# Kernel optimization log

Hardware: AMD Instinct MI355X
Metric: run time of the kernel (lower is better)

## Reference

```python
import jax, jax.numpy as jnp
import numpy as np

B, S, D, H = 2, 2048, 1024, 16
HD = D // H  # head_dim = 64


def setup_inputs() -> dict:
    key = jax.random.key(0)
    ks = jax.random.split(key, 5)
    scale = 1.0 / np.sqrt(D)
    return {
        "x": jax.random.normal(ks[0], (B, S, D), dtype=jnp.float32),
        "attention_mask": jnp.zeros((B, 1, 1, S), dtype=jnp.float32),
        "Wq": jax.random.normal(ks[1], (D, D), dtype=jnp.float32) * scale,
        "Wk": jax.random.normal(ks[2], (D, D), dtype=jnp.float32) * scale,
        "Wv": jax.random.normal(ks[3], (D, D), dtype=jnp.float32) * scale,
        "Wo": jax.random.normal(ks[4], (D, D), dtype=jnp.float32) * scale,
    }


def reference(x, attention_mask, Wq, Wk, Wv, Wo):
    # nn.Linear applies x @ W.T; weights here stored as [out, in]
    q = jnp.einsum("bsd,ed->bse", x, Wq).reshape(B, S, H, HD).transpose(0, 2, 1, 3)
    k = jnp.einsum("bsd,ed->bse", x, Wk).reshape(B, S, H, HD).transpose(0, 2, 1, 3)
    v = jnp.einsum("bsd,ed->bse", x, Wv).reshape(B, S, H, HD).transpose(0, 2, 1, 3)
    scores = jnp.einsum("bhqd,bhkd->bhqk", q, k) / jnp.sqrt(jnp.float32(HD))
    scores = scores + attention_mask  # additive mask, broadcasts [B,1,1,S]
    attn = jax.nn.softmax(scores, axis=-1)  # dropout p=0 (eval) -> identity
    ctx = jnp.einsum("bhqk,bhkd->bhqd", attn, v)
    ctx = ctx.transpose(0, 2, 1, 3).reshape(B, S, D)
    out = jnp.einsum("bsd,ed->bse", ctx, Wo)
    return out
```

## Files before the change

kernel.cpp:

```cpp
#include <hip/hip_runtime.h>
#include <hip/hip_bf16.h>
#include <cstdint>
#include <cstddef>


#define B_  2
#define S_  2048
#define D_  1024
#define H_  16
#define HD_ 64

typedef __bf16 bf16x8 __attribute__((ext_vector_type(8)));
typedef __bf16 bf16x4 __attribute__((ext_vector_type(4)));
typedef float  f32x4  __attribute__((ext_vector_type(4)));

__device__ __forceinline__ void async16(const __bf16* g, const __bf16* l) {
  __builtin_amdgcn_global_load_lds(
      (const __attribute__((address_space(1))) void*)(uintptr_t)g,
      (__attribute__((address_space(3))) void*)(uint32_t)(uintptr_t)l,
      16, 0, 0);
}

__device__ __forceinline__ unsigned cvt_pk_bf16(float lo, float hi) {
  unsigned r;
  asm("v_cvt_pk_bf16_f32 %0, %1, %2" : "=v"(r) : "v"(lo), "v"(hi));
  return r;
}

__global__ __launch_bounds__(256) void cvt_all(const float* __restrict__ x,
    const float* __restrict__ wq, const float* __restrict__ wk,
    const float* __restrict__ wv, const float* __restrict__ wo,
    __bf16* __restrict__ xb, __bf16* __restrict__ wqb, __bf16* __restrict__ wkb,
    __bf16* __restrict__ wvb, __bf16* __restrict__ wob) {
  const int sel = blockIdx.y;
  const float* src; __bf16* dst; int n;
  if      (sel == 0) { src = x;  dst = xb;  n = B_ * S_ * D_; }
  else if (sel == 1) { src = wq; dst = wqb; n = D_ * D_; }
  else if (sel == 2) { src = wk; dst = wkb; n = D_ * D_; }
  else if (sel == 3) { src = wv; dst = wvb; n = D_ * D_; }
  else               { src = wo; dst = wob; n = D_ * D_; }
  for (int i = blockIdx.x * 256 + threadIdx.x; i * 4 < n; i += gridDim.x * 256) {
    const float4 v = *(const float4*)(src + (size_t)i * 4);
    bf16x4 o;
    o[0] = (__bf16)v.x; o[1] = (__bf16)v.y; o[2] = (__bf16)v.z; o[3] = (__bf16)v.w;
    *(bf16x4*)(dst + (size_t)i * 4) = o;
  }
}

__global__ __launch_bounds__(512, 4) void qkv_gemm(const __bf16* __restrict__ xb,
                                                   const __bf16* __restrict__ wqkv,
                                                   __bf16* __restrict__ qkv) {
  __shared__ __align__(16) char smem[65536];
  __bf16* cs = (__bf16*)smem;

  const int lin = blockIdx.y * 24 + blockIdx.x;
  const int xcd = lin & 7, slot = lin >> 3;
  const int mi = xcd >> 2, ni = xcd & 3;
  const int mB = mi * 16 + slot / 6;
  const int nB = ni * 6  + slot % 6;
  const int m0  = mB * 128;
  const int sel = nB >> 3;
  const int n0s = (nB & 7) * 128;
  const int n0w = nB * 128;
  constexpr int K = D_, N = D_;
  constexpr size_t NTE = (size_t)B_ * S_ * D_;

  const int tid  = threadIdx.x, lane = tid & 63, wave = tid >> 6;
  const int l15  = lane & 15,   quad = lane >> 4;
  const int wr   = wave >> 1,   wc   = wave & 1;

  const int e0 = (wave * 2 + 0) * 512 + lane * 8;
  const int e1 = (wave * 2 + 1) * 512 + lane * 8;
  const int r0 = e0 >> 6, c0 = e0 & 63, r1 = e1 >> 6, c1 = e1 & 63;

  f32x4 acc[2][4] = {};

  {
    __bf16* As = (__bf16*)(smem);
    __bf16* Bs = (__bf16*)(smem + 16384);
    async16(xb   + (size_t)(m0  + r0) * K + c0, As + (wave * 2 + 0) * 512);
    async16(xb   + (size_t)(m0  + r1) * K + c1, As + (wave * 2 + 1) * 512);
    async16(wqkv + (size_t)(n0w + r0) * K + c0, Bs + (wave * 2 + 0) * 512);
    async16(wqkv + (size_t)(n0w + r1) * K + c1, Bs + (wave * 2 + 1) * 512);
  }
  __syncthreads();

  for (int t = 0; t < K / 64; ++t) {
    const int cur = t & 1;
    if (t + 1 < K / 64) {
      const int k0 = (t + 1) * 64;
      __bf16* As = (__bf16*)(smem + (cur ^ 1) * 32768);
      __bf16* Bs = (__bf16*)(smem + (cur ^ 1) * 32768 + 16384);
      async16(xb   + (size_t)(m0  + r0) * K + k0 + c0, As + (wave * 2 + 0) * 512);
      async16(xb   + (size_t)(m0  + r1) * K + k0 + c1, As + (wave * 2 + 1) * 512);
      async16(wqkv + (size_t)(n0w + r0) * K + k0 + c0, Bs + (wave * 2 + 0) * 512);
      async16(wqkv + (size_t)(n0w + r1) * K + k0 + c1, Bs + (wave * 2 + 1) * 512);
    }
    const __bf16* As = (const __bf16*)(smem + cur * 32768);
    const __bf16* Bs = (const __bf16*)(smem + cur * 32768 + 16384);
#pragma unroll
    for (int kk = 0; kk < 2; ++kk) {
      bf16x8 af[2], bfv[4];
#pragma unroll
      for (int rt = 0; rt < 2; ++rt)
        af[rt] = *(const bf16x8*)(As + (wr * 32 + rt * 16 + l15) * 64 + kk * 32 + quad * 8);
#pragma unroll
      for (int ct = 0; ct < 4; ++ct)
        bfv[ct] = *(const bf16x8*)(Bs + (wc * 64 + ct * 16 + l15) * 64 + kk * 32 + quad * 8);
#pragma unroll
      for (int rt = 0; rt < 2; ++rt)
#pragma unroll
        for (int ct = 0; ct < 4; ++ct)
          acc[rt][ct] = __builtin_amdgcn_mfma_f32_16x16x32_bf16(af[rt], bfv[ct], acc[rt][ct], 0, 0, 0);
    }
    __syncthreads();
  }

  const int b  = m0 >> 11;
  const int s0 = m0 & (S_ - 1);
  __bf16* vtb = qkv + 2 * NTE;
#pragma unroll
  for (int pass = 0; pass < 2; ++pass) {
    __syncthreads();
    if ((wave >> 2) == pass) {
#pragma unroll
      for (int rt = 0; rt < 2; ++rt)
#pragma unroll
        for (int ct = 0; ct < 4; ++ct)
#pragma unroll
          for (int r = 0; r < 4; ++r)
            cs[((wr & 1) * 32 + rt * 16 + quad * 4 + r) * 136 + wc * 64 + ct * 16 + l15] =
                (__bf16)acc[rt][ct][r];
    }
    __syncthreads();
    if (sel < 2) {
      __bf16* C = qkv + (size_t)sel * NTE;
      const int rr = tid >> 3, cb = (tid & 7) * 16;
      const bf16x8 v0 = *(const bf16x8*)(cs + rr * 136 + cb);
      const bf16x8 v1 = *(const bf16x8*)(cs + rr * 136 + cb + 8);
      *(bf16x8*)(C + (size_t)(m0 + pass * 64 + rr) * N + n0s + cb)     = v0;
      *(bf16x8*)(C + (size_t)(m0 + pass * 64 + rr) * N + n0s + cb + 8) = v1;
    } else {
      const int e_loc = tid >> 2, sh = (tid & 3) * 16;
      __bf16* dst = vtb + (size_t)(b * 1024 + n0s + e_loc) * S_ + s0 + pass * 64 + sh;
#pragma unroll
      for (int p2 = 0; p2 < 2; ++p2) {
        bf16x8 v;
#pragma unroll
        for (int j = 0; j < 8; ++j)
          v[j] = cs[(sh + p2 * 8 + j) * 136 + e_loc];
        *(bf16x8*)(dst + p2 * 8) = v;
      }
    }
  }
}

__global__ __launch_bounds__(512, 4) void o_gemm(const __bf16* __restrict__ cb,
                                                 const __bf16* __restrict__ wo,
                                                 float* __restrict__ out) {
  __shared__ __align__(16) char smem[49152];
  const int lin = blockIdx.y * 8 + blockIdx.x;
  const int xcd = lin & 7, slot = lin >> 3;
  const int mi = xcd >> 1, ni = xcd & 1;
  const int mB = mi * 16 + (slot >> 2);
  const int nB = ni * 4  + (slot & 3);
  const int m0 = mB * 64, n0 = nB * 128;
  constexpr int K = D_, N = D_;
  const int tid  = threadIdx.x, lane = tid & 63, wave = tid >> 6;
  const int l15  = lane & 15,   quad = lane >> 4;
  const int wr   = wave >> 2,   wc   = wave & 3;

  const int ea  = wave * 512 + lane * 8;
  const int ra  = ea >> 6, ca = ea & 63;
  const int eb0 = (wave * 2 + 0) * 512 + lane * 8;
  const int eb1 = (wave * 2 + 1) * 512 + lane * 8;
  const int rb0 = eb0 >> 6, cb0 = eb0 & 63, rb1 = eb1 >> 6, cb1 = eb1 & 63;

  f32x4 acc[2][2] = {};
  {
    __bf16* As = (__bf16*)(smem);
    __bf16* Bs = (__bf16*)(smem + 8192);
    async16(cb + (size_t)(m0 + ra)  * K + ca,  As + wave * 512);
    async16(wo + (size_t)(n0 + rb0) * K + cb0, Bs + (wave * 2 + 0) * 512);
    async16(wo + (size_t)(n0 + rb1) * K + cb1, Bs + (wave * 2 + 1) * 512);
  }
  __syncthreads();

  for (int t = 0; t < K / 64; ++t) {
    const int cur = t & 1;
    if (t + 1 < K / 64) {
      const int k0 = (t + 1) * 64;
      __bf16* As = (__bf16*)(smem + (cur ^ 1) * 24576);
      __bf16* Bs = (__bf16*)(smem + (cur ^ 1) * 24576 + 8192);
      async16(cb + (size_t)(m0 + ra)  * K + k0 + ca,  As + wave * 512);
      async16(wo + (size_t)(n0 + rb0) * K + k0 + cb0, Bs + (wave * 2 + 0) * 512);
      async16(wo + (size_t)(n0 + rb1) * K + k0 + cb1, Bs + (wave * 2 + 1) * 512);
    }
    const __bf16* As = (const __bf16*)(smem + cur * 24576);
    const __bf16* Bs = (const __bf16*)(smem + cur * 24576 + 8192);
#pragma unroll
    for (int kk = 0; kk < 2; ++kk) {
      bf16x8 af[2], bfv[2];
#pragma unroll
      for (int rt = 0; rt < 2; ++rt)
        af[rt] = *(const bf16x8*)(As + (wr * 32 + rt * 16 + l15) * 64 + kk * 32 + quad * 8);
#pragma unroll
      for (int ct = 0; ct < 2; ++ct)
        bfv[ct] = *(const bf16x8*)(Bs + (wc * 32 + ct * 16 + l15) * 64 + kk * 32 + quad * 8);
#pragma unroll
      for (int rt = 0; rt < 2; ++rt)
#pragma unroll
        for (int ct = 0; ct < 2; ++ct)
          acc[rt][ct] = __builtin_amdgcn_mfma_f32_16x16x32_bf16(af[rt], bfv[ct], acc[rt][ct], 0, 0, 0);
    }
    __syncthreads();
  }
#pragma unroll
  for (int rt = 0; rt < 2; ++rt)
#pragma unroll
    for (int ct = 0; ct < 2; ++ct)
#pragma unroll
      for (int r = 0; r < 4; ++r) {
        const int row = m0 + wr * 32 + rt * 16 + quad * 4 + r;
        const int col = n0 + wc * 32 + ct * 16 + l15;
        out[(size_t)row * N + col] = acc[rt][ct][r];
      }
}

__global__ __launch_bounds__(512, 4) void attn2(const __bf16* __restrict__ Q,
                                                const __bf16* __restrict__ K,
                                                const __bf16* __restrict__ Vt,
                                                const float* __restrict__ mask,
                                                __bf16* __restrict__ O) {
  constexpr int LKT = 72, LVT = 136;
  __shared__ __align__(16) __bf16 kt[2][128 * LKT];
  __shared__ __align__(16) __bf16 vt[2][64 * LVT];
  __shared__ __align__(16) float  mfull[S_];

  const int tid  = threadIdx.x, lane = tid & 63, wave = tid >> 6;
  const int l15  = lane & 15,   quad = lane >> 4;
  const int b = blockIdx.z, h = blockIdx.y, q0 = blockIdx.x * 128;
  const size_t base   = (size_t)b * S_ * D_ + h * HD_;
  const size_t vtbase = (size_t)(b * H_ + h) * HD_ * S_;
  const int qw = q0 + wave * 16;
  constexpr float LOG2E = 1.44269504088896340736f;
  constexpr float SC    = 0.125f * LOG2E;
  constexpr int  NT     = S_ / 128;

  const int idx0 = tid,        kr0 = idx0 >> 3, kc0 = (idx0 & 7) * 8;
  const int idx1 = 512 + tid,  kr1 = idx1 >> 3, kc1 = (idx1 & 7) * 8;
  const int vr0 = idx0 >> 4, vc0 = (idx0 & 15) * 8;
  const int vr1 = idx1 >> 4, vc1 = (idx1 & 15) * 8;

  bf16x8 qf[2];
#pragma unroll
  for (int kb = 0; kb < 2; ++kb)
    qf[kb] = *(const bf16x8*)(Q + base + (size_t)(qw + l15) * D_ + kb * 32 + quad * 8);

  bf16x8 ones;
#pragma unroll
  for (int j = 0; j < 8; ++j) ones[j] = (__bf16)1.0f;

  float m_run = -1e30f;
  f32x4 oacc[4] = {};
  f32x4 lacc   = {};

  bf16x8 rk0, rk1, rv0, rv1;
  rk0 = *(const bf16x8*)(K + base + (size_t)kr0 * D_ + kc0);
  rk1 = *(const bf16x8*)(K + base + (size_t)kr1 * D_ + kc1);
  rv0 = *(const bf16x8*)(Vt + vtbase + (size_t)vr0 * S_ + vc0);
  rv1 = *(const bf16x8*)(Vt + vtbase + (size_t)vr1 * S_ + vc1);
#pragma unroll
  for (int i = 0; i < S_ / 512; ++i)
    mfull[i * 512 + tid] = mask[(size_t)b * S_ + i * 512 + tid] * LOG2E;
  *(bf16x8*)(&kt[0][kr0 * LKT + kc0]) = rk0;
  *(bf16x8*)(&kt[0][kr1 * LKT + kc1]) = rk1;
  *(bf16x8*)(&vt[0][vr0 * LVT + vc0]) = rv0;
  *(bf16x8*)(&vt[0][vr1 * LVT + vc1]) = rv1;
  if (NT > 1) {
    rk0 = *(const bf16x8*)(K + base + (size_t)(128 + kr0) * D_ + kc0);
    rk1 = *(const bf16x8*)(K + base + (size_t)(128 + kr1) * D_ + kc1);
    rv0 = *(const bf16x8*)(Vt + vtbase + (size_t)vr0 * S_ + 128 + vc0);
    rv1 = *(const bf16x8*)(Vt + vtbase + (size_t)vr1 * S_ + 128 + vc1);
  }
  __syncthreads();

  for (int t = 0; t < NT; ++t) {
    const int cur = t & 1;
    const int t0  = t * 128;
    const __bf16* ktb = &kt[cur][0];
    const __bf16* vtb = &vt[cur][0];

    if (t + 1 < NT) {
      const int nxt = cur ^ 1;
      *(bf16x8*)(&kt[nxt][kr0 * LKT + kc0]) = rk0;
      *(bf16x8*)(&kt[nxt][kr1 * LKT + kc1]) = rk1;
      *(bf16x8*)(&vt[nxt][vr0 * LVT + vc0]) = rv0;
      *(bf16x8*)(&vt[nxt][vr1 * LVT + vc1]) = rv1;
    }
    if (t + 2 < NT) {
      const int tn = t0 + 256;
      rk0 = *(const bf16x8*)(K + base + (size_t)(tn + kr0) * D_ + kc0);
      rk1 = *(const bf16x8*)(K + base + (size_t)(tn + kr1) * D_ + kc1);
      rv0 = *(const bf16x8*)(Vt + vtbase + (size_t)vr0 * S_ + tn + vc0);
      rv1 = *(const bf16x8*)(Vt + vtbase + (size_t)vr1 * S_ + tn + vc1);
    }

    f32x4 sacc[8] = {};
    __builtin_amdgcn_s_setprio(1);
#pragma unroll
    for (int kti = 0; kti < 8; ++kti) {
      const __bf16* kr = ktb + (kti * 16 + l15) * LKT + quad * 8;
      const bf16x8 a0 = *(const bf16x8*)(kr);
      const bf16x8 a1 = *(const bf16x8*)(kr + 32);
      sacc[kti] = __builtin_amdgcn_mfma_f32_16x16x32_bf16(a0, qf[0], sacc[kti], 0, 0, 0);
      sacc[kti] = __builtin_amdgcn_mfma_f32_16x16x32_bf16(a1, qf[1], sacc[kti], 0, 0, 0);
    }
    __builtin_amdgcn_s_setprio(0);

    f32x4 tm4;
#pragma unroll
    for (int r = 0; r < 4; ++r) tm4[r] = -1e30f;
#pragma unroll
    for (int kti = 0; kti < 8; ++kti) {
      const f32x4 mv = *(const f32x4*)(mfull + t0 + kti * 16 + quad * 4);
#pragma unroll
      for (int r = 0; r < 4; ++r) {
        sacc[kti][r] = sacc[kti][r] * SC + mv[r];
        tm4[r] = fmaxf(tm4[r], sacc[kti][r]);
      }
    }
    float tm = fmaxf(fmaxf(tm4[0], tm4[1]), fmaxf(tm4[2], tm4[3]));
    tm = fmaxf(tm, __shfl_xor(tm, 16));
    tm = fmaxf(tm, __shfl_xor(tm, 32));

    if (!__all(tm <= m_run + 8.f)) {
      const float mnew  = fmaxf(m_run, tm);
      const float alpha = __builtin_amdgcn_exp2f(m_run - mnew);
      m_run = mnew;
#pragma unroll
      for (int r = 0; r < 4; ++r) {
        const float aR = __shfl(alpha, quad * 4 + r);
        lacc[r] *= aR;
#pragma unroll
        for (int nt = 0; nt < 4; ++nt) oacc[nt][r] *= aR;
      }
    }

#pragma unroll
    for (int kb = 0; kb < 4; ++kb) {
      unsigned dd[2][2];
#pragma unroll
      for (int kk = 0; kk < 2; ++kk) {
        const int kti = 2 * kb + kk;
        float p[4];
#pragma unroll
        for (int r = 0; r < 4; ++r)
          p[r] = __builtin_amdgcn_exp2f(sacc[kti][r] - m_run);
        dd[kk][0] = cvt_pk_bf16(p[0], p[1]);
        dd[kk][1] = cvt_pk_bf16(p[2], p[3]);
      }
      unsigned a0 = dd[0][0], b0 = dd[1][0], a1 = dd[0][1], b1 = dd[1][1];
      asm("v_permlane32_swap_b32 %0, %1" : "+v"(a0), "+v"(b0));
      asm("v_permlane16_swap_b32 %0, %1" : "+v"(a0), "+v"(b0));
      asm("v_permlane32_swap_b32 %0, %1" : "+v"(a1), "+v"(b1));
      asm("v_permlane16_swap_b32 %0, %1" : "+v"(a1), "+v"(b1));
      union { unsigned u[4]; bf16x8 v; } pw;
      pw.u[0] = a0; pw.u[1] = a1; pw.u[2] = b0; pw.u[3] = b1;
      const bf16x8 pa = pw.v;
      __builtin_amdgcn_s_setprio(1);
      lacc = __builtin_amdgcn_mfma_f32_16x16x32_bf16(pa, ones, lacc, 0, 0, 0);
#pragma unroll
      for (int nt = 0; nt < 4; ++nt) {
        const bf16x8 vf = *(const bf16x8*)(vtb + (nt * 16 + l15) * LVT + kb * 32 + quad * 8);
        oacc[nt] = __builtin_amdgcn_mfma_f32_16x16x32_bf16(pa, vf, oacc[nt], 0, 0, 0);
      }
      __builtin_amdgcn_s_setprio(0);
    }

    __syncthreads();
  }

#pragma unroll
  for (int r = 0; r < 4; ++r) {
    const float inv = 1.0f / lacc[r];
    const int row = qw + quad * 4 + r;
#pragma unroll
    for (int nt = 0; nt < 4; ++nt)
      O[base + (size_t)row * D_ + nt * 16 + l15] = (__bf16)(oacc[nt][r] * inv);
  }
}

extern "C" void kernel_launch(void* const* d_in, const int* in_sizes, int n_in,
                              void* d_out, int out_size, void* d_ws, size_t ws_size,
                              hipStream_t stream) {
  const float* x    = (const float*)d_in[0];
  const float* mask = (const float*)d_in[1];
  const float* Wq   = (const float*)d_in[2];
  const float* Wk   = (const float*)d_in[3];
  const float* Wv   = (const float*)d_in[4];
  const float* Wo   = (const float*)d_in[5];

  char* ws = (char*)d_ws;
  const size_t MB = 1ull << 20;
  const size_t NT = (size_t)B_ * S_ * D_;
  __bf16* xb  = (__bf16*)(ws);
  __bf16* wqb = (__bf16*)(ws + 8 * MB);
  __bf16* wkb = (__bf16*)(ws + 10 * MB);
  __bf16* wvb = (__bf16*)(ws + 12 * MB);
  __bf16* wob = (__bf16*)(ws + 14 * MB);
  __bf16* qkv = (__bf16*)(ws + 16 * MB);
  __bf16* qb  = qkv;
  __bf16* kb  = qkv + NT;
  __bf16* vtb = qkv + 2 * NT;
  __bf16* cb  = xb;

  cvt_all<<<dim3(1024, 5), 256, 0, stream>>>(x, Wq, Wk, Wv, Wo, xb, wqb, wkb, wvb, wob);
  qkv_gemm<<<dim3(24, 32), 512, 0, stream>>>(xb, wqb, qkv);
  attn2<<<dim3(S_ / 128, H_, B_), 512, 0, stream>>>(qb, kb, vtb, mask, cb);
  o_gemm<<<dim3(8, 64), 512, 0, stream>>>(cb, wob, (float*)d_out);
}
```

Baseline: 200.1 us.

## Enlarge QKV GEMM tiles to 256x256 and shrink o_gemm blocks to 256 threads

The QKV projection GEMM moves from 128x128 tiles on 768 blocks to 256x256 tiles on 192 blocks. It uses 128KB of LDS and each wave holds an 8x4 accumulator grid, which raises operand reuse per LDS load. The epilogue now writes out in four passes. o_gemm runs with 4 waves per block instead of 8, each wave covering a 32x64 output. Risks: only 192 blocks for 256 CUs, so many CUs sit idle, plus high register pressure and one block per CU with less latency hiding.

```diff
diff --git a/kernel.cpp b/kernel.cpp
--- a/kernel.cpp
+++ b/kernel.cpp
@@ -47,41 +47,38 @@
   }
 }
 
-__global__ __launch_bounds__(512, 4) void qkv_gemm(const __bf16* __restrict__ xb,
+__global__ __launch_bounds__(512, 1) void qkv_gemm(const __bf16* __restrict__ xb,
                                                    const __bf16* __restrict__ wqkv,
                                                    __bf16* __restrict__ qkv) {
-  __shared__ __align__(16) char smem[65536];
+  __shared__ __align__(16) char smem[131072];
   __bf16* cs = (__bf16*)smem;
 
-  const int lin = blockIdx.y * 24 + blockIdx.x;
+  const int lin = blockIdx.y * 12 + blockIdx.x;
   const int xcd = lin & 7, slot = lin >> 3;
-  const int mi = xcd >> 2, ni = xcd & 3;
-  const int mB = mi * 16 + slot / 6;
-  const int nB = ni * 6  + slot % 6;
-  const int m0  = mB * 128;
-  const int sel = nB >> 3;
-  const int n0s = (nB & 7) * 128;
-  const int n0w = nB * 128;
+  const int mB = (xcd >> 2) * 8 + slot / 3;
+  const int nB = (xcd & 3) * 3 + slot % 3;
+  const int m0  = mB * 256;
+  const int sel = nB >> 2;
+  const int n0s = (nB & 3) * 256;
+  const int n0w = nB * 256;
   constexpr int K = D_, N = D_;
   constexpr size_t NTE = (size_t)B_ * S_ * D_;
 
   const int tid  = threadIdx.x, lane = tid & 63, wave = tid >> 6;
   const int l15  = lane & 15,   quad = lane >> 4;
-  const int wr   = wave >> 1,   wc   = wave & 1;
-
-  const int e0 = (wave * 2 + 0) * 512 + lane * 8;
-  const int e1 = (wave * 2 + 1) * 512 + lane * 8;
-  const int r0 = e0 >> 6, c0 = e0 & 63, r1 = e1 >> 6, c1 = e1 & 63;
-
-  f32x4 acc[2][4] = {};
+  const int wr   = wave >> 2,   wc   = wave & 3;
+  const int row8 = tid >> 3, col8 = (tid & 7) * 8;
+
+  f32x4 acc[8][4] = {};
 
   {
     __bf16* As = (__bf16*)(smem);
-    __bf16* Bs = (__bf16*)(smem + 16384);
-    async16(xb   + (size_t)(m0  + r0) * K + c0, As + (wave * 2 + 0) * 512);
-    async16(xb   + (size_t)(m0  + r1) * K + c1, As + (wave * 2 + 1) * 512);
-    async16(wqkv + (size_t)(n0w + r0) * K + c0, Bs + (wave * 2 + 0) * 512);
-    async16(wqkv + (size_t)(n0w + r1) * K + c1, Bs + (wave * 2 + 1) * 512);
+    __bf16* Bs = (__bf16*)(smem + 32768);
+#pragma unroll
+    for (int i = 0; i < 4; ++i) {
+      async16(xb   + (size_t)(m0  + i * 64 + row8) * K + col8, As + i * 4096 + wave * 512);
+      async16(wqkv + (size_t)(n0w + i * 64 + row8) * K + col8, Bs + i * 4096 + wave * 512);
+    }
   }
   __syncthreads();
 
@@ -89,29 +86,29 @@
     const int cur = t & 1;
     if (t + 1 < K / 64) {
       const int k0 = (t + 1) * 64;
-      __bf16* As = (__bf16*)(smem + (cur ^ 1) * 32768);
-      __bf16* Bs = (__bf16*)(smem + (cur ^ 1) * 32768 + 16384);
-      async16(xb   + (size_t)(m0  + r0) * K + k0 + c0, As + (wave * 2 + 0) * 512);
-      async16(xb   + (size_t)(m0  + r1) * K + k0 + c1, As + (wave * 2 + 1) * 512);
-      async16(wqkv + (size_t)(n0w + r0) * K + k0 + c0, Bs + (wave * 2 + 0) * 512);
-      async16(wqkv + (size_t)(n0w + r1) * K + k0 + c1, Bs + (wave * 2 + 1) * 512);
-    }
-    const __bf16* As = (const __bf16*)(smem + cur * 32768);
-    const __bf16* Bs = (const __bf16*)(smem + cur * 32768 + 16384);
+      __bf16* As = (__bf16*)(smem + (cur ^ 1) * 65536);
+      __bf16* Bs = (__bf16*)(smem + (cur ^ 1) * 65536 + 32768);
+#pragma unroll
+      for (int i = 0; i < 4; ++i) {
+        async16(xb   + (size_t)(m0  + i * 64 + row8) * K + k0 + col8, As + i * 4096 + wave * 512);
+        async16(wqkv + (size_t)(n0w + i * 64 + row8) * K + k0 + col8, Bs + i * 4096 + wave * 512);
+      }
+    }
+    const __bf16* As = (const __bf16*)(smem + cur * 65536);
+    const __bf16* Bs = (const __bf16*)(smem + cur * 65536 + 32768);
 #pragma unroll
     for (int kk = 0; kk < 2; ++kk) {
-      bf16x8 af[2], bfv[4];
-#pragma unroll
-      for (int rt = 0; rt < 2; ++rt)
-        af[rt] = *(const bf16x8*)(As + (wr * 32 + rt * 16 + l15) * 64 + kk * 32 + quad * 8);
+      bf16x8 bfv[4];
 #pragma unroll
       for (int ct = 0; ct < 4; ++ct)
         bfv[ct] = *(const bf16x8*)(Bs + (wc * 64 + ct * 16 + l15) * 64 + kk * 32 + quad * 8);
 #pragma unroll
-      for (int rt = 0; rt < 2; ++rt)
+      for (int rt = 0; rt < 8; ++rt) {
+        const bf16x8 af = *(const bf16x8*)(As + (wr * 128 + rt * 16 + l15) * 64 + kk * 32 + quad * 8);
 #pragma unroll
         for (int ct = 0; ct < 4; ++ct)
-          acc[rt][ct] = __builtin_amdgcn_mfma_f32_16x16x32_bf16(af[rt], bfv[ct], acc[rt][ct], 0, 0, 0);
+          acc[rt][ct] = __builtin_amdgcn_mfma_f32_16x16x32_bf16(af, bfv[ct], acc[rt][ct], 0, 0, 0);
+      }
     }
     __syncthreads();
   }
@@ -120,44 +117,46 @@
   const int s0 = m0 & (S_ - 1);
   __bf16* vtb = qkv + 2 * NTE;
 #pragma unroll
-  for (int pass = 0; pass < 2; ++pass) {
+  for (int pass = 0; pass < 4; ++pass) {
     __syncthreads();
-    if ((wave >> 2) == pass) {
-#pragma unroll
-      for (int rt = 0; rt < 2; ++rt)
+    if (wr == (pass >> 1)) {
+      const int rtb = (pass & 1) * 4;
+#pragma unroll
+      for (int rt = 0; rt < 4; ++rt)
 #pragma unroll
         for (int ct = 0; ct < 4; ++ct)
 #pragma unroll
           for (int r = 0; r < 4; ++r)
-            cs[((wr & 1) * 32 + rt * 16 + quad * 4 + r) * 136 + wc * 64 + ct * 16 + l15] =
-                (__bf16)acc[rt][ct][r];
+            cs[(rt * 16 + quad * 4 + r) * 264 + wc * 64 + ct * 16 + l15] =
+                (__bf16)acc[rtb + rt][ct][r];
     }
     __syncthreads();
     if (sel < 2) {
       __bf16* C = qkv + (size_t)sel * NTE;
-      const int rr = tid >> 3, cb = (tid & 7) * 16;
-      const bf16x8 v0 = *(const bf16x8*)(cs + rr * 136 + cb);
-      const bf16x8 v1 = *(const bf16x8*)(cs + rr * 136 + cb + 8);
-      *(bf16x8*)(C + (size_t)(m0 + pass * 64 + rr) * N + n0s + cb)     = v0;
-      *(bf16x8*)(C + (size_t)(m0 + pass * 64 + rr) * N + n0s + cb + 8) = v1;
+      const int rr = tid >> 3, cb = (tid & 7) * 32;
+#pragma unroll
+      for (int j2 = 0; j2 < 4; ++j2) {
+        const bf16x8 v = *(const bf16x8*)(cs + rr * 264 + cb + j2 * 8);
+        *(bf16x8*)(C + (size_t)(m0 + pass * 64 + rr) * N + n0s + cb + j2 * 8) = v;
+      }
     } else {
-      const int e_loc = tid >> 2, sh = (tid & 3) * 16;
+      const int e_loc = tid >> 1, sh = (tid & 1) * 32;
       __bf16* dst = vtb + (size_t)(b * 1024 + n0s + e_loc) * S_ + s0 + pass * 64 + sh;
 #pragma unroll
-      for (int p2 = 0; p2 < 2; ++p2) {
+      for (int j2 = 0; j2 < 4; ++j2) {
         bf16x8 v;
 #pragma unroll
         for (int j = 0; j < 8; ++j)
-          v[j] = cs[(sh + p2 * 8 + j) * 136 + e_loc];
-        *(bf16x8*)(dst + p2 * 8) = v;
-      }
-    }
-  }
-}
-
-__global__ __launch_bounds__(512, 4) void o_gemm(const __bf16* __restrict__ cb,
-                                                 const __bf16* __restrict__ wo,
-                                                 float* __restrict__ out) {
+          v[j] = cs[(sh + j2 * 8 + j) * 264 + e_loc];
+        *(bf16x8*)(dst + j2 * 8) = v;
+      }
+    }
+  }
+}
+
+__global__ __launch_bounds__(256) void o_gemm(const __bf16* __restrict__ cb,
+                                              const __bf16* __restrict__ wo,
+                                              float* __restrict__ out) {
   __shared__ __align__(16) char smem[49152];
   const int lin = blockIdx.y * 8 + blockIdx.x;
   const int xcd = lin & 7, slot = lin >> 3;
@@ -168,21 +167,19 @@
   constexpr int K = D_, N = D_;
   const int tid  = threadIdx.x, lane = tid & 63, wave = tid >> 6;
   const int l15  = lane & 15,   quad = lane >> 4;
-  const int wr   = wave >> 2,   wc   = wave & 3;
-
-  const int ea  = wave * 512 + lane * 8;
-  const int ra  = ea >> 6, ca = ea & 63;
-  const int eb0 = (wave * 2 + 0) * 512 + lane * 8;
-  const int eb1 = (wave * 2 + 1) * 512 + lane * 8;
-  const int rb0 = eb0 >> 6, cb0 = eb0 & 63, rb1 = eb1 >> 6, cb1 = eb1 & 63;
-
-  f32x4 acc[2][2] = {};
+  const int wr   = wave >> 1,   wc   = wave & 1;
+  const int row8 = tid >> 3, col8 = (tid & 7) * 8;
+
+  f32x4 acc[2][4] = {};
   {
     __bf16* As = (__bf16*)(smem);
     __bf16* Bs = (__bf16*)(smem + 8192);
-    async16(cb + (size_t)(m0 + ra)  * K + ca,  As + wave * 512);
-    async16(wo + (size_t)(n0 + rb0) * K + cb0, Bs + (wave * 2 + 0) * 512);
-    async16(wo + (size_t)(n0 + rb1) * K + cb1, Bs + (wave * 2 + 1) * 512);
+#pragma unroll
+    for (int i = 0; i < 2; ++i)
+      async16(cb + (size_t)(m0 + i * 32 + row8) * K + col8, As + i * 2048 + wave * 512);
+#pragma unroll
+    for (int i = 0; i < 4; ++i)
+      async16(wo + (size_t)(n0 + i * 32 + row8) * K + col8, Bs + i * 2048 + wave * 512);
   }
   __syncthreads();
 
@@ -192,25 +189,28 @@
       const int k0 = (t + 1) * 64;
       __bf16* As = (__bf16*)(smem + (cur ^ 1) * 24576);
       __bf16* Bs = (__bf16*)(smem + (cur ^ 1) * 24576 + 8192);
-      async16(cb + (size_t)(m0 + ra)  * K + k0 + ca,  As + wave * 512);
-      async16(wo + (size_t)(n0 + rb0) * K + k0 + cb0, Bs + (wave * 2 + 0) * 512);
-      async16(wo + (size_t)(n0 + rb1) * K + k0 + cb1, Bs + (wave * 2 + 1) * 512);
+#pragma unroll
+      for (int i = 0; i < 2; ++i)
+        async16(cb + (size_t)(m0 + i * 32 + row8) * K + k0 + col8, As + i * 2048 + wave * 512);
+#pragma unroll
+      for (int i = 0; i < 4; ++i)
+        async16(wo + (size_t)(n0 + i * 32 + row8) * K + k0 + col8, Bs + i * 2048 + wave * 512);
     }
     const __bf16* As = (const __bf16*)(smem + cur * 24576);
     const __bf16* Bs = (const __bf16*)(smem + cur * 24576 + 8192);
 #pragma unroll
     for (int kk = 0; kk < 2; ++kk) {
-      bf16x8 af[2], bfv[2];
+      bf16x8 af[2], bfv[4];
 #pragma unroll
       for (int rt = 0; rt < 2; ++rt)
         af[rt] = *(const bf16x8*)(As + (wr * 32 + rt * 16 + l15) * 64 + kk * 32 + quad * 8);
 #pragma unroll
-      for (int ct = 0; ct < 2; ++ct)
-        bfv[ct] = *(const bf16x8*)(Bs + (wc * 32 + ct * 16 + l15) * 64 + kk * 32 + quad * 8);
+      for (int ct = 0; ct < 4; ++ct)
+        bfv[ct] = *(const bf16x8*)(Bs + (wc * 64 + ct * 16 + l15) * 64 + kk * 32 + quad * 8);
 #pragma unroll
       for (int rt = 0; rt < 2; ++rt)
 #pragma unroll
-        for (int ct = 0; ct < 2; ++ct)
+        for (int ct = 0; ct < 4; ++ct)
           acc[rt][ct] = __builtin_amdgcn_mfma_f32_16x16x32_bf16(af[rt], bfv[ct], acc[rt][ct], 0, 0, 0);
     }
     __syncthreads();
@@ -218,11 +218,11 @@
 #pragma unroll
   for (int rt = 0; rt < 2; ++rt)
 #pragma unroll
-    for (int ct = 0; ct < 2; ++ct)
+    for (int ct = 0; ct < 4; ++ct)
 #pragma unroll
       for (int r = 0; r < 4; ++r) {
         const int row = m0 + wr * 32 + rt * 16 + quad * 4 + r;
-        const int col = n0 + wc * 32 + ct * 16 + l15;
+        const int col = n0 + wc * 64 + ct * 16 + l15;
         out[(size_t)row * N + col] = acc[rt][ct][r];
       }
 }
@@ -416,7 +416,7 @@
   __bf16* cb  = xb;
 
   cvt_all<<<dim3(1024, 5), 256, 0, stream>>>(x, Wq, Wk, Wv, Wo, xb, wqb, wkb, wvb, wob);
-  qkv_gemm<<<dim3(24, 32), 512, 0, stream>>>(xb, wqb, qkv);
+  qkv_gemm<<<dim3(12, 16), 512, 0, stream>>>(xb, wqb, qkv);
   attn2<<<dim3(S_ / 128, H_, B_), 512, 0, stream>>>(qb, kb, vtb, mask, cb);
-  o_gemm<<<dim3(8, 64), 512, 0, stream>>>(cb, wob, (float*)d_out);
-}
+  o_gemm<<<dim3(8, 64), 256, 0, stream>>>(cb, wob, (float*)d_out);
+}
```

Result: no change. 197.0 us (-1.6%).
